# Kernel optimization log

Hardware: AMD Instinct MI355X
Metric: run time of the kernel (lower is better)

Reference implementation:

```python
import jax, jax.numpy as jnp
import numpy as np

EMBED = 1024
MLP = 2048
N_EXPERTS = 8
TOP_K = 2


def setup_inputs() -> dict:
    key = jax.random.key(0)
    ks = jax.random.split(key, 5)
    scale_e = 1.0 / np.sqrt(EMBED)
    scale_m = 1.0 / np.sqrt(MLP)
    x = jax.random.normal(ks[0], (4, 2048, EMBED), dtype=jnp.float32)
    gate_w = jax.random.normal(ks[1], (EMBED, N_EXPERTS), dtype=jnp.float32) * scale_e
    w1 = jax.random.normal(ks[2], (N_EXPERTS, EMBED, MLP), dtype=jnp.float32) * scale_e
    w3 = jax.random.normal(ks[3], (N_EXPERTS, EMBED, MLP), dtype=jnp.float32) * scale_e
    w2 = jax.random.normal(ks[4], (N_EXPERTS, MLP, EMBED), dtype=jnp.float32) * scale_m
    return {"x": x, "gate_w": gate_w, "w1": w1, "w2": w2, "w3": w3}


def reference(x, gate_w, w1, w2, w3):
    B, S, D = x.shape
    xf = x.reshape(-1, D)  # [T, D] tokens
    # Router: softmax over experts, top-k select, renormalize selected weights
    router_logits = xf @ gate_w                      # [T, E]
    routing_weights = jax.nn.softmax(router_logits, axis=-1)
    sel_w, sel_e = jax.lax.top_k(routing_weights, TOP_K)  # [T, K]
    sel_w = sel_w / jnp.sum(sel_w, axis=-1, keepdims=True)
    out = jnp.zeros_like(xf)
    # Loop over the small fixed expert set; tokens not routed to expert e get
    # coefficient 0, matching the gather/scatter-add combine of the original.
    for e in range(N_EXPERTS):
        coef = jnp.sum(jnp.where(sel_e == e, sel_w, 0.0), axis=-1)  # [T]
        h = jax.nn.silu(xf @ w1[e]) * (xf @ w3[e])                  # [T, Mlp] SwiGLU
        out = out + coef[:, None] * (h @ w2[e])                     # [T, D]
    return out.reshape(B, S, D)
```

## Files before the change

kernel.cpp:

```cpp
#include <hip/hip_runtime.h>

#define EMBED 1024
#define MLP   2048
#define NE    8
#define NTOK  8192
#define RMAX  (2*NTOK + NE*128)

typedef _Float16 f16x8 __attribute__((ext_vector_type(8)));
typedef _Float16 f16x4 __attribute__((ext_vector_type(4)));
typedef float    f32x4 __attribute__((ext_vector_type(4)));

__device__ __forceinline__ void async_copy16(const void* g, void* l) {
  __builtin_amdgcn_global_load_lds(
      (const __attribute__((address_space(1))) unsigned int*)g,
      (__attribute__((address_space(3))) unsigned int*)l, 16, 0, 0);
}

__global__ __launch_bounds__(256) void router_kernel(
    const float* __restrict__ x, const float* __restrict__ gw,
    int* __restrict__ sel_e, float* __restrict__ sel_w, int* __restrict__ counts)
{
  __shared__ float gwt[NE * EMBED];
  __shared__ int cnt[NE];
  int tid = threadIdx.x;
  for (int idx = tid; idx < NE * EMBED; idx += 256) {
    int i = idx >> 3, e = idx & 7;
    gwt[e * EMBED + i] = gw[idx];
  }
  if (tid < NE) cnt[tid] = 0;
  __syncthreads();

  int lane = tid & 63, wv = tid >> 6;
  int t = blockIdx.x * 4 + wv;
  const float4* xr = (const float4*)(x + (size_t)t * EMBED);
  const float4* gt4 = (const float4*)gwt;
  float acc[NE];
  #pragma unroll
  for (int e = 0; e < NE; ++e) acc[e] = 0.f;
  #pragma unroll
  for (int c = 0; c < 4; ++c) {
    float4 xv = xr[c * 64 + lane];
    #pragma unroll
    for (int e = 0; e < NE; ++e) {
      float4 gv = gt4[e * 256 + c * 64 + lane];
      acc[e] += xv.x * gv.x + xv.y * gv.y + xv.z * gv.z + xv.w * gv.w;
    }
  }
  #pragma unroll
  for (int off = 1; off < 64; off <<= 1) {
    #pragma unroll
    for (int e = 0; e < NE; ++e) acc[e] += __shfl_xor(acc[e], off);
  }
  if (lane == 0) {
    int e0 = 0; float l0 = acc[0];
    #pragma unroll
    for (int e = 1; e < NE; ++e) if (acc[e] > l0) { l0 = acc[e]; e0 = e; }
    int e1 = -1; float l1 = -1e30f;
    #pragma unroll
    for (int e = 0; e < NE; ++e) if (e != e0 && acc[e] > l1) { l1 = acc[e]; e1 = e; }
    float w0 = 1.f / (1.f + expf(l1 - l0));
    sel_e[2 * t] = e0;     sel_w[2 * t] = w0;
    sel_e[2 * t + 1] = e1; sel_w[2 * t + 1] = 1.f - w0;
    atomicAdd(&cnt[e0], 1); atomicAdd(&cnt[e1], 1);
  }
  __syncthreads();
  if (tid < NE && cnt[tid]) atomicAdd(&counts[tid], cnt[tid]);
}

__global__ void offsets_kernel(const int* __restrict__ counts,
                               int* __restrict__ offs, int* __restrict__ cursor)
{
  if (threadIdx.x == 0) {
    int o = 0;
    for (int e = 0; e < NE; ++e) {
      offs[e] = o; cursor[e] = o;
      o += (counts[e] + 127) & ~127;
    }
    offs[NE] = o;
  }
}

__global__ __launch_bounds__(256) void assign_kernel(
    const int* __restrict__ sel_e, const float* __restrict__ sel_w,
    int* __restrict__ cursor, int* __restrict__ rowtok, float* __restrict__ rowcoef)
{
  int t = blockIdx.x * 256 + threadIdx.x;
  int lane = threadIdx.x & 63;
  #pragma unroll
  for (int k = 0; k < 2; ++k) {
    int e = sel_e[2 * t + k];
    float w = sel_w[2 * t + k];
    for (int xch = 0; xch < NE; ++xch) {
      unsigned long long m = __ballot(e == xch);
      if (e == xch) {
        int leader = __ffsll((unsigned long long)m) - 1;
        int base = 0;
        if (lane == leader) base = atomicAdd(&cursor[xch], (int)__popcll(m));
        base = __shfl(base, leader);
        int pos = base + (int)__popcll(m & ((1ull << lane) - 1));
        rowtok[pos] = t;
        rowcoef[pos] = w;
      }
    }
  }
}

__global__ __launch_bounds__(256) void gather_kernel(
    const float* __restrict__ x, const int* __restrict__ rowtok,
    _Float16* __restrict__ xg)
{
  int r = blockIdx.x;
  int tok = rowtok[r];
  int t4 = threadIdx.x * 4;
  _Float16* dst = xg + (size_t)r * EMBED + t4;
  if (tok >= 0) {
    float4 v = *(const float4*)(x + (size_t)tok * EMBED + t4);
    f16x4 h; h.x = (_Float16)v.x; h.y = (_Float16)v.y; h.z = (_Float16)v.z; h.w = (_Float16)v.w;
    *(f16x4*)dst = h;
  } else {
    f16x4 z = {(_Float16)0.f, (_Float16)0.f, (_Float16)0.f, (_Float16)0.f};
    *(f16x4*)dst = z;
  }
}

__global__ __launch_bounds__(256) void transpose_cast_kernel(
    const float* __restrict__ in, _Float16* __restrict__ out, int K, int N)
{
  const float* src = in + (size_t)blockIdx.z * K * N;
  _Float16* dst = out + (size_t)blockIdx.z * K * N;
  int k0 = blockIdx.x * 64, n0 = blockIdx.y * 64;
  __shared__ float tile[64][65];
  int t = threadIdx.x;
  int r = t >> 4, c4 = (t & 15) * 4;
  #pragma unroll
  for (int i = 0; i < 4; ++i) {
    float4 v = *(const float4*)(src + (size_t)(k0 + r + 16 * i) * N + n0 + c4);
    tile[r + 16 * i][c4 + 0] = v.x;
    tile[r + 16 * i][c4 + 1] = v.y;
    tile[r + 16 * i][c4 + 2] = v.z;
    tile[r + 16 * i][c4 + 3] = v.w;
  }
  __syncthreads();
  int kk8 = (t & 7) * 8, nIdx = t >> 3;
  #pragma unroll
  for (int i = 0; i < 2; ++i) {
    int n = nIdx + 32 * i;
    f16x8 h;
    #pragma unroll
    for (int j = 0; j < 8; ++j) h[j] = (_Float16)tile[kk8 + j][n];
    *(f16x8*)(dst + (size_t)(n0 + n) * K + k0 + kk8) = h;
  }
}

__device__ __forceinline__ int resolve_expert(const int* __restrict__ offs, int r0)
{
  int e = 0;
  #pragma unroll
  for (int q = 0; q < NE - 1; ++q) if (r0 >= offs[q + 1]) e = q + 1;
  return e;
}

__device__ __forceinline__ const _Float16* frag_addr(const _Float16* buf, int row, int quad)
{
  return buf + row * 32 + ((quad ^ ((row >> 1) & 3)) << 3);
}

__global__ __launch_bounds__(256, 2) void gemm1_kernel(
    const _Float16* __restrict__ xg, const _Float16* __restrict__ w1t,
    const _Float16* __restrict__ w3t, const float* __restrict__ rowcoef,
    const int* __restrict__ offs, _Float16* __restrict__ hb)
{
  int r0 = blockIdx.x * 128;
  if (r0 >= offs[NE]) return;
  int e = resolve_expert(offs, r0);
  int n0 = blockIdx.y * 128;
  const _Float16* B1 = w1t + (size_t)e * MLP * EMBED;
  const _Float16* B3 = w3t + (size_t)e * MLP * EMBED;

  __shared__ __align__(16) _Float16 As[128 * 32];
  __shared__ __align__(16) _Float16 Bs1[128 * 32];
  __shared__ __align__(16) _Float16 Bs3[128 * 32];

  int tid = threadIdx.x, lane = tid & 63, wv = tid >> 6;
  int wm = (wv & 1) << 6, wn = (wv >> 1) << 6;
  int l16 = lane & 15, quad = lane >> 4;

  f32x4 acc1[4][4], acc3[4][4];
  f32x4 z4 = {0.f, 0.f, 0.f, 0.f};
  #pragma unroll
  for (int i = 0; i < 4; ++i)
    #pragma unroll
    for (int j = 0; j < 4; ++j) { acc1[i][j] = z4; acc3[i][j] = z4; }

  for (int kk = 0; kk < EMBED; kk += 32) {
    __syncthreads();
    #pragma unroll
    for (int p = 0; p < 2; ++p) {
      int c = p * 256 + tid;
      int row = c >> 2, kqp = c & 3;
      int kql = kqp ^ ((row >> 1) & 3);
      size_t gof = (size_t)(r0 + row) * EMBED + kk + kql * 8;
      size_t gofB = (size_t)(n0 + row) * EMBED + kk + kql * 8;
      int lof = (p * 256 + wv * 64) * 8;
      async_copy16(xg + gof,  As  + lof);
      async_copy16(B1 + gofB, Bs1 + lof);
      async_copy16(B3 + gofB, Bs3 + lof);
    }
    __syncthreads();
    f16x8 af[4], b1f[4], b3f[4];
    #pragma unroll
    for (int i = 0; i < 4; ++i)
      af[i] = *(const f16x8*)frag_addr(As, wm + 16 * i + l16, quad);
    #pragma unroll
    for (int j = 0; j < 4; ++j) {
      b1f[j] = *(const f16x8*)frag_addr(Bs1, wn + 16 * j + l16, quad);
      b3f[j] = *(const f16x8*)frag_addr(Bs3, wn + 16 * j + l16, quad);
    }
    #pragma unroll
    for (int i = 0; i < 4; ++i)
      #pragma unroll
      for (int j = 0; j < 4; ++j) {
        acc1[i][j] = __builtin_amdgcn_mfma_f32_16x16x32_f16(af[i], b1f[j], acc1[i][j], 0, 0, 0);
        acc3[i][j] = __builtin_amdgcn_mfma_f32_16x16x32_f16(af[i], b3f[j], acc3[i][j], 0, 0, 0);
      }
  }

  #pragma unroll
  for (int i = 0; i < 4; ++i) {
    int mb = r0 + wm + 16 * i + quad * 4;
    float cf[4];
    #pragma unroll
    for (int rg = 0; rg < 4; ++rg) cf[rg] = rowcoef[mb + rg];
    #pragma unroll
    for (int j = 0; j < 4; ++j) {
      int col = n0 + wn + 16 * j + l16;
      #pragma unroll
      for (int rg = 0; rg < 4; ++rg) {
        float g = acc1[i][j][rg], u = acc3[i][j][rg];
        float h = g * u * cf[rg] / (1.f + __expf(-g));
        hb[(size_t)(mb + rg) * MLP + col] = (_Float16)h;
      }
    }
  }
}

__global__ __launch_bounds__(256, 2) void gemm2_kernel(
    const _Float16* __restrict__ hb, const _Float16* __restrict__ w2t,
    const int* __restrict__ rowtok, const int* __restrict__ offs,
    float* __restrict__ out)
{
  int r0 = blockIdx.x * 128;
  if (r0 >= offs[NE]) return;
  int e = resolve_expert(offs, r0);
  int n0 = blockIdx.y * 128;
  const _Float16* B = w2t + (size_t)e * EMBED * MLP;

  __shared__ __align__(16) _Float16 As[128 * 32];
  __shared__ __align__(16) _Float16 Bs[128 * 32];

  int tid = threadIdx.x, lane = tid & 63, wv = tid >> 6;
  int wm = (wv & 1) << 6, wn = (wv >> 1) << 6;
  int l16 = lane & 15, quad = lane >> 4;

  f32x4 acc[4][4];
  f32x4 z4 = {0.f, 0.f, 0.f, 0.f};
  #pragma unroll
  for (int i = 0; i < 4; ++i)
    #pragma unroll
    for (int j = 0; j < 4; ++j) acc[i][j] = z4;

  for (int kk = 0; kk < MLP; kk += 32) {
    __syncthreads();
    #pragma unroll
    for (int p = 0; p < 2; ++p) {
      int c = p * 256 + tid;
      int row = c >> 2, kqp = c & 3;
      int kql = kqp ^ ((row >> 1) & 3);
      size_t gofA = (size_t)(r0 + row) * MLP + kk + kql * 8;
      size_t gofB = (size_t)(n0 + row) * MLP + kk + kql * 8;
      int lof = (p * 256 + wv * 64) * 8;
      async_copy16(hb + gofA, As + lof);
      async_copy16(B  + gofB, Bs + lof);
    }
    __syncthreads();
    f16x8 af[4], bf[4];
    #pragma unroll
    for (int i = 0; i < 4; ++i)
      af[i] = *(const f16x8*)frag_addr(As, wm + 16 * i + l16, quad);
    #pragma unroll
    for (int j = 0; j < 4; ++j)
      bf[j] = *(const f16x8*)frag_addr(Bs, wn + 16 * j + l16, quad);
    #pragma unroll
    for (int i = 0; i < 4; ++i)
      #pragma unroll
      for (int j = 0; j < 4; ++j)
        acc[i][j] = __builtin_amdgcn_mfma_f32_16x16x32_f16(af[i], bf[j], acc[i][j], 0, 0, 0);
  }

  #pragma unroll
  for (int i = 0; i < 4; ++i) {
    int mb = r0 + wm + 16 * i + quad * 4;
    int tk[4];
    #pragma unroll
    for (int rg = 0; rg < 4; ++rg) tk[rg] = rowtok[mb + rg];
    #pragma unroll
    for (int j = 0; j < 4; ++j) {
      int col = n0 + wn + 16 * j + l16;
      #pragma unroll
      for (int rg = 0; rg < 4; ++rg)
        if (tk[rg] >= 0)
          atomicAdd(out + (size_t)tk[rg] * EMBED + col, acc[i][j][rg]);
    }
  }
}

extern "C" void kernel_launch(void* const* d_in, const int* in_sizes, int n_in,
                              void* d_out, int out_size, void* d_ws, size_t ws_size,
                              hipStream_t stream)
{
  (void)in_sizes; (void)n_in; (void)ws_size;
  const float* x  = (const float*)d_in[0];
  const float* gw = (const float*)d_in[1];
  const float* w1 = (const float*)d_in[2];
  const float* w2 = (const float*)d_in[3];
  const float* w3 = (const float*)d_in[4];
  float* out = (float*)d_out;
  char* ws = (char*)d_ws;

  size_t o = 0;
  auto alloc = [&](size_t bytes) { size_t r = o; o = (o + bytes + 255) & ~255ULL; return r; };
  const size_t wbytes = (size_t)NE * MLP * EMBED * 2;
  _Float16* w1t = (_Float16*)(ws + alloc(wbytes));
  _Float16* w3t = (_Float16*)(ws + alloc(wbytes));
  _Float16* w2t = (_Float16*)(ws + alloc(wbytes));
  _Float16* xg  = (_Float16*)(ws + alloc((size_t)RMAX * EMBED * 2));
  _Float16* hb  = (_Float16*)(ws + alloc((size_t)RMAX * MLP * 2));
  int*   rowtok  = (int*)(ws + alloc((size_t)RMAX * 4));
  float* rowcoef = (float*)(ws + alloc((size_t)RMAX * 4));
  int*   sel_e   = (int*)(ws + alloc((size_t)2 * NTOK * 4));
  float* sel_w   = (float*)(ws + alloc((size_t)2 * NTOK * 4));
  int*   meta    = (int*)(ws + alloc(256));
  int* counts = meta;
  int* offs   = meta + 8;
  int* cursor = meta + 17;

  hipMemsetAsync(out, 0, (size_t)out_size * 4, stream);
  hipMemsetAsync(meta, 0, 256, stream);
  hipMemsetAsync(rowtok, 0xFF, (size_t)RMAX * 4, stream);
  hipMemsetAsync(rowcoef, 0, (size_t)RMAX * 4, stream);

  transpose_cast_kernel<<<dim3(EMBED / 64, MLP / 64, NE), 256, 0, stream>>>(w1, w1t, EMBED, MLP);
  transpose_cast_kernel<<<dim3(EMBED / 64, MLP / 64, NE), 256, 0, stream>>>(w3, w3t, EMBED, MLP);
  transpose_cast_kernel<<<dim3(MLP / 64, EMBED / 64, NE), 256, 0, stream>>>(w2, w2t, MLP, EMBED);

  router_kernel<<<NTOK / 4, 256, 0, stream>>>(x, gw, sel_e, sel_w, counts);
  offsets_kernel<<<1, 64, 0, stream>>>(counts, offs, cursor);
  assign_kernel<<<NTOK / 256, 256, 0, stream>>>(sel_e, sel_w, cursor, rowtok, rowcoef);
  gather_kernel<<<RMAX, 256, 0, stream>>>(x, rowtok, xg);

  gemm1_kernel<<<dim3(RMAX / 128, MLP / 128), 256, 0, stream>>>(xg, w1t, w3t, rowcoef, offs, hb);
  gemm2_kernel<<<dim3(RMAX / 128, EMBED / 128), 256, 0, stream>>>(hb, w2t, rowtok, offs, out);
}
```

Before: 678.4 us.

## Load GEMM A operands directly from global, deepen K tile, replace atomics with combine

The expert GEMMs now read A fragments straight from global memory into registers instead of staging them in LDS, and the K step grows to 64 with a new XOR swizzle for the B tiles. The atomic scatter-add in the second GEMM is replaced by an fp16 store into a per-row buffer, followed by a combine kernel that sums each token's two expert rows through an inverse index. The three weight transpose launches are merged into one. This is meant to remove atomic contention, the output memset and LDS traffic for A, at the cost of uncoalesced global A loads, an extra pass over the output, and fp16 rounding of the partial expert outputs.

Result: slower. 709.6 us (+4.6%).

```diff
diff --git a/kernel.cpp b/kernel.cpp
--- a/kernel.cpp
+++ b/kernel.cpp
@@ -5,6 +5,7 @@
 #define NE    8
 #define NTOK  8192
 #define RMAX  (2*NTOK + NE*128)
+#define BK    64
 
 typedef _Float16 f16x8 __attribute__((ext_vector_type(8)));
 typedef _Float16 f16x4 __attribute__((ext_vector_type(4)));
@@ -82,7 +83,8 @@
 
 __global__ __launch_bounds__(256) void assign_kernel(
     const int* __restrict__ sel_e, const float* __restrict__ sel_w,
-    int* __restrict__ cursor, int* __restrict__ rowtok, float* __restrict__ rowcoef)
+    int* __restrict__ cursor, int* __restrict__ rowtok, float* __restrict__ rowcoef,
+    int* __restrict__ inv)
 {
   int t = blockIdx.x * 256 + threadIdx.x;
   int lane = threadIdx.x & 63;
@@ -100,6 +102,7 @@
         int pos = base + (int)__popcll(m & ((1ull << lane) - 1));
         rowtok[pos] = t;
         rowcoef[pos] = w;
+        inv[2 * t + k] = pos;
       }
     }
   }
@@ -123,22 +126,34 @@
   }
 }
 
-__global__ __launch_bounds__(256) void transpose_cast_kernel(
-    const float* __restrict__ in, _Float16* __restrict__ out, int K, int N)
-{
-  const float* src = in + (size_t)blockIdx.z * K * N;
-  _Float16* dst = out + (size_t)blockIdx.z * K * N;
-  int k0 = blockIdx.x * 64, n0 = blockIdx.y * 64;
-  __shared__ float tile[64][65];
+__global__ __launch_bounds__(256) void transpose_all_kernel(
+    const float* __restrict__ w1, const float* __restrict__ w3,
+    const float* __restrict__ w2, _Float16* __restrict__ w1t,
+    _Float16* __restrict__ w3t, _Float16* __restrict__ w2t)
+{
+  int id = blockIdx.x;
+  int mat = id >> 12;
+  int rr = id & 4095;
+  int e = rr >> 9, tile = rr & 511;
+  const float* src; _Float16* dst; int K, N;
+  if (mat == 0)      { src = w1; dst = w1t; K = EMBED; N = MLP; }
+  else if (mat == 1) { src = w3; dst = w3t; K = EMBED; N = MLP; }
+  else               { src = w2; dst = w2t; K = MLP;   N = EMBED; }
+  int nx = K >> 6;
+  int k0 = (tile % nx) * 64, n0 = (tile / nx) * 64;
+  src += (size_t)e * K * N;
+  dst += (size_t)e * K * N;
+
+  __shared__ float tilebuf[64][65];
   int t = threadIdx.x;
   int r = t >> 4, c4 = (t & 15) * 4;
   #pragma unroll
   for (int i = 0; i < 4; ++i) {
     float4 v = *(const float4*)(src + (size_t)(k0 + r + 16 * i) * N + n0 + c4);
-    tile[r + 16 * i][c4 + 0] = v.x;
-    tile[r + 16 * i][c4 + 1] = v.y;
-    tile[r + 16 * i][c4 + 2] = v.z;
-    tile[r + 16 * i][c4 + 3] = v.w;
+    tilebuf[r + 16 * i][c4 + 0] = v.x;
+    tilebuf[r + 16 * i][c4 + 1] = v.y;
+    tilebuf[r + 16 * i][c4 + 2] = v.z;
+    tilebuf[r + 16 * i][c4 + 3] = v.w;
   }
   __syncthreads();
   int kk8 = (t & 7) * 8, nIdx = t >> 3;
@@ -147,7 +162,7 @@
     int n = nIdx + 32 * i;
     f16x8 h;
     #pragma unroll
-    for (int j = 0; j < 8; ++j) h[j] = (_Float16)tile[kk8 + j][n];
+    for (int j = 0; j < 8; ++j) h[j] = (_Float16)tilebuf[kk8 + j][n];
     *(f16x8*)(dst + (size_t)(n0 + n) * K + k0 + kk8) = h;
   }
 }
@@ -160,9 +175,10 @@
   return e;
 }
 
-__device__ __forceinline__ const _Float16* frag_addr(const _Float16* buf, int row, int quad)
-{
-  return buf + row * 32 + ((quad ^ ((row >> 1) & 3)) << 3);
+__device__ __forceinline__ const _Float16* bfrag_addr(const _Float16* buf, int row,
+                                                      int s, int quad)
+{
+  return buf + row * BK + ((((s << 2) + quad) ^ (row & 7)) << 3);
 }
 
 __global__ __launch_bounds__(256, 2) void gemm1_kernel(
@@ -177,14 +193,18 @@
   const _Float16* B1 = w1t + (size_t)e * MLP * EMBED;
   const _Float16* B3 = w3t + (size_t)e * MLP * EMBED;
 
-  __shared__ __align__(16) _Float16 As[128 * 32];
-  __shared__ __align__(16) _Float16 Bs1[128 * 32];
-  __shared__ __align__(16) _Float16 Bs3[128 * 32];
+  __shared__ __align__(16) _Float16 Bs1[128 * BK];
+  __shared__ __align__(16) _Float16 Bs3[128 * BK];
 
   int tid = threadIdx.x, lane = tid & 63, wv = tid >> 6;
   int wm = (wv & 1) << 6, wn = (wv >> 1) << 6;
   int l16 = lane & 15, quad = lane >> 4;
 
+  const _Float16* Arow[4];
+  #pragma unroll
+  for (int i = 0; i < 4; ++i)
+    Arow[i] = xg + (size_t)(r0 + wm + 16 * i + l16) * EMBED + quad * 8;
+
   f32x4 acc1[4][4], acc3[4][4];
   f32x4 z4 = {0.f, 0.f, 0.f, 0.f};
   #pragma unroll
@@ -192,37 +212,42 @@
     #pragma unroll
     for (int j = 0; j < 4; ++j) { acc1[i][j] = z4; acc3[i][j] = z4; }
 
-  for (int kk = 0; kk < EMBED; kk += 32) {
+  for (int kk = 0; kk < EMBED; kk += BK) {
     __syncthreads();
     #pragma unroll
-    for (int p = 0; p < 2; ++p) {
+    for (int p = 0; p < 4; ++p) {
       int c = p * 256 + tid;
-      int row = c >> 2, kqp = c & 3;
-      int kql = kqp ^ ((row >> 1) & 3);
-      size_t gof = (size_t)(r0 + row) * EMBED + kk + kql * 8;
-      size_t gofB = (size_t)(n0 + row) * EMBED + kk + kql * 8;
+      int row = c >> 3, cp = c & 7;
+      int cl = cp ^ (row & 7);
+      size_t gof = (size_t)(n0 + row) * EMBED + kk + cl * 8;
       int lof = (p * 256 + wv * 64) * 8;
-      async_copy16(xg + gof,  As  + lof);
-      async_copy16(B1 + gofB, Bs1 + lof);
-      async_copy16(B3 + gofB, Bs3 + lof);
-    }
+      async_copy16(B1 + gof, Bs1 + lof);
+      async_copy16(B3 + gof, Bs3 + lof);
+    }
+    f16x8 af[2][4];
+    #pragma unroll
+    for (int s = 0; s < 2; ++s)
+      #pragma unroll
+      for (int i = 0; i < 4; ++i)
+        af[s][i] = *(const f16x8*)(Arow[i] + kk + s * 32);
     __syncthreads();
-    f16x8 af[4], b1f[4], b3f[4];
-    #pragma unroll
-    for (int i = 0; i < 4; ++i)
-      af[i] = *(const f16x8*)frag_addr(As, wm + 16 * i + l16, quad);
-    #pragma unroll
-    for (int j = 0; j < 4; ++j) {
-      b1f[j] = *(const f16x8*)frag_addr(Bs1, wn + 16 * j + l16, quad);
-      b3f[j] = *(const f16x8*)frag_addr(Bs3, wn + 16 * j + l16, quad);
-    }
-    #pragma unroll
-    for (int i = 0; i < 4; ++i)
+    #pragma unroll
+    for (int s = 0; s < 2; ++s) {
+      f16x8 b1f[4], b3f[4];
       #pragma unroll
       for (int j = 0; j < 4; ++j) {
-        acc1[i][j] = __builtin_amdgcn_mfma_f32_16x16x32_f16(af[i], b1f[j], acc1[i][j], 0, 0, 0);
-        acc3[i][j] = __builtin_amdgcn_mfma_f32_16x16x32_f16(af[i], b3f[j], acc3[i][j], 0, 0, 0);
+        int row = wn + 16 * j + l16;
+        b1f[j] = *(const f16x8*)bfrag_addr(Bs1, row, s, quad);
+        b3f[j] = *(const f16x8*)bfrag_addr(Bs3, row, s, quad);
       }
+      #pragma unroll
+      for (int i = 0; i < 4; ++i)
+        #pragma unroll
+        for (int j = 0; j < 4; ++j) {
+          acc1[i][j] = __builtin_amdgcn_mfma_f32_16x16x32_f16(af[s][i], b1f[j], acc1[i][j], 0, 0, 0);
+          acc3[i][j] = __builtin_amdgcn_mfma_f32_16x16x32_f16(af[s][i], b3f[j], acc3[i][j], 0, 0, 0);
+        }
+    }
   }
 
   #pragma unroll
@@ -246,8 +271,7 @@
 
 __global__ __launch_bounds__(256, 2) void gemm2_kernel(
     const _Float16* __restrict__ hb, const _Float16* __restrict__ w2t,
-    const int* __restrict__ rowtok, const int* __restrict__ offs,
-    float* __restrict__ out)
+    const int* __restrict__ offs, _Float16* __restrict__ hb2)
 {
   int r0 = blockIdx.x * 128;
   if (r0 >= offs[NE]) return;
@@ -255,13 +279,17 @@
   int n0 = blockIdx.y * 128;
   const _Float16* B = w2t + (size_t)e * EMBED * MLP;
 
-  __shared__ __align__(16) _Float16 As[128 * 32];
-  __shared__ __align__(16) _Float16 Bs[128 * 32];
+  __shared__ __align__(16) _Float16 Bs[128 * BK];
 
   int tid = threadIdx.x, lane = tid & 63, wv = tid >> 6;
   int wm = (wv & 1) << 6, wn = (wv >> 1) << 6;
   int l16 = lane & 15, quad = lane >> 4;
 
+  const _Float16* Arow[4];
+  #pragma unroll
+  for (int i = 0; i < 4; ++i)
+    Arow[i] = hb + (size_t)(r0 + wm + 16 * i + l16) * MLP + quad * 8;
+
   f32x4 acc[4][4];
   f32x4 z4 = {0.f, 0.f, 0.f, 0.f};
   #pragma unroll
@@ -269,56 +297,73 @@
     #pragma unroll
     for (int j = 0; j < 4; ++j) acc[i][j] = z4;
 
-  for (int kk = 0; kk < MLP; kk += 32) {
+  for (int kk = 0; kk < MLP; kk += BK) {
     __syncthreads();
     #pragma unroll
-    for (int p = 0; p < 2; ++p) {
+    for (int p = 0; p < 4; ++p) {
       int c = p * 256 + tid;
-      int row = c >> 2, kqp = c & 3;
-      int kql = kqp ^ ((row >> 1) & 3);
-      size_t gofA = (size_t)(r0 + row) * MLP + kk + kql * 8;
-      size_t gofB = (size_t)(n0 + row) * MLP + kk + kql * 8;
+      int row = c >> 3, cp = c & 7;
+      int cl = cp ^ (row & 7);
+      size_t gof = (size_t)(n0 + row) * MLP + kk + cl * 8;
       int lof = (p * 256 + wv * 64) * 8;
-      async_copy16(hb + gofA, As + lof);
-      async_copy16(B  + gofB, Bs + lof);
-    }
+      async_copy16(B + gof, Bs + lof);
+    }
+    f16x8 af[2][4];
+    #pragma unroll
+    for (int s = 0; s < 2; ++s)
+      #pragma unroll
+      for (int i = 0; i < 4; ++i)
+        af[s][i] = *(const f16x8*)(Arow[i] + kk + s * 32);
     __syncthreads();
-    f16x8 af[4], bf[4];
-    #pragma unroll
-    for (int i = 0; i < 4; ++i)
-      af[i] = *(const f16x8*)frag_addr(As, wm + 16 * i + l16, quad);
-    #pragma unroll
-    for (int j = 0; j < 4; ++j)
-      bf[j] = *(const f16x8*)frag_addr(Bs, wn + 16 * j + l16, quad);
-    #pragma unroll
-    for (int i = 0; i < 4; ++i)
+    #pragma unroll
+    for (int s = 0; s < 2; ++s) {
+      f16x8 bf[4];
       #pragma unroll
       for (int j = 0; j < 4; ++j)
-        acc[i][j] = __builtin_amdgcn_mfma_f32_16x16x32_f16(af[i], bf[j], acc[i][j], 0, 0, 0);
+        bf[j] = *(const f16x8*)bfrag_addr(Bs, wn + 16 * j + l16, s, quad);
+      #pragma unroll
+      for (int i = 0; i < 4; ++i)
+        #pragma unroll
+        for (int j = 0; j < 4; ++j)
+          acc[i][j] = __builtin_amdgcn_mfma_f32_16x16x32_f16(af[s][i], bf[j], acc[i][j], 0, 0, 0);
+    }
   }
 
   #pragma unroll
   for (int i = 0; i < 4; ++i) {
     int mb = r0 + wm + 16 * i + quad * 4;
-    int tk[4];
-    #pragma unroll
-    for (int rg = 0; rg < 4; ++rg) tk[rg] = rowtok[mb + rg];
     #pragma unroll
     for (int j = 0; j < 4; ++j) {
       int col = n0 + wn + 16 * j + l16;
       #pragma unroll
       for (int rg = 0; rg < 4; ++rg)
-        if (tk[rg] >= 0)
-          atomicAdd(out + (size_t)tk[rg] * EMBED + col, acc[i][j][rg]);
-    }
-  }
+        hb2[(size_t)(mb + rg) * EMBED + col] = (_Float16)acc[i][j][rg];
+    }
+  }
+}
+
+__global__ __launch_bounds__(256) void combine_kernel(
+    const _Float16* __restrict__ hb2, const int* __restrict__ inv,
+    float* __restrict__ out)
+{
+  int t = blockIdx.x;
+  int d = threadIdx.x * 4;
+  int p0 = inv[2 * t], p1 = inv[2 * t + 1];
+  f16x4 a = *(const f16x4*)(hb2 + (size_t)p0 * EMBED + d);
+  f16x4 b = *(const f16x4*)(hb2 + (size_t)p1 * EMBED + d);
+  float4 r;
+  r.x = (float)a.x + (float)b.x;
+  r.y = (float)a.y + (float)b.y;
+  r.z = (float)a.z + (float)b.z;
+  r.w = (float)a.w + (float)b.w;
+  *(float4*)(out + (size_t)t * EMBED + d) = r;
 }
 
 extern "C" void kernel_launch(void* const* d_in, const int* in_sizes, int n_in,
                               void* d_out, int out_size, void* d_ws, size_t ws_size,
                               hipStream_t stream)
 {
-  (void)in_sizes; (void)n_in; (void)ws_size;
+  (void)in_sizes; (void)n_in; (void)ws_size; (void)out_size;
   const float* x  = (const float*)d_in[0];
   const float* gw = (const float*)d_in[1];
   const float* w1 = (const float*)d_in[2];
@@ -339,25 +384,25 @@
   float* rowcoef = (float*)(ws + alloc((size_t)RMAX * 4));
   int*   sel_e   = (int*)(ws + alloc((size_t)2 * NTOK * 4));
   float* sel_w   = (float*)(ws + alloc((size_t)2 * NTOK * 4));
+  int*   inv     = (int*)(ws + alloc((size_t)2 * NTOK * 4));
   int*   meta    = (int*)(ws + alloc(256));
   int* counts = meta;
   int* offs   = meta + 8;
   int* cursor = meta + 17;
-
-  hipMemsetAsync(out, 0, (size_t)out_size * 4, stream);
+  _Float16* hb2 = xg;
+
   hipMemsetAsync(meta, 0, 256, stream);
   hipMemsetAsync(rowtok, 0xFF, (size_t)RMAX * 4, stream);
   hipMemsetAsync(rowcoef, 0, (size_t)RMAX * 4, stream);
 
-  transpose_cast_kernel<<<dim3(EMBED / 64, MLP / 64, NE), 256, 0, stream>>>(w1, w1t, EMBED, MLP);
-  transpose_cast_kernel<<<dim3(EMBED / 64, MLP / 64, NE), 256, 0, stream>>>(w3, w3t, EMBED, MLP);
-  transpose_cast_kernel<<<dim3(MLP / 64, EMBED / 64, NE), 256, 0, stream>>>(w2, w2t, MLP, EMBED);
+  transpose_all_kernel<<<3 * 4096, 256, 0, stream>>>(w1, w3, w2, w1t, w3t, w2t);
 
   router_kernel<<<NTOK / 4, 256, 0, stream>>>(x, gw, sel_e, sel_w, counts);
   offsets_kernel<<<1, 64, 0, stream>>>(counts, offs, cursor);
-  assign_kernel<<<NTOK / 256, 256, 0, stream>>>(sel_e, sel_w, cursor, rowtok, rowcoef);
+  assign_kernel<<<NTOK / 256, 256, 0, stream>>>(sel_e, sel_w, cursor, rowtok, rowcoef, inv);
   gather_kernel<<<RMAX, 256, 0, stream>>>(x, rowtok, xg);
 
   gemm1_kernel<<<dim3(RMAX / 128, MLP / 128), 256, 0, stream>>>(xg, w1t, w3t, rowcoef, offs, hb);
-  gemm2_kernel<<<dim3(RMAX / 128, EMBED / 128), 256, 0, stream>>>(hb, w2t, rowtok, offs, out);
-}
+  gemm2_kernel<<<dim3(RMAX / 128, EMBED / 128), 256, 0, stream>>>(hb, w2t, offs, hb2);
+  combine_kernel<<<NTOK, 256, 0, stream>>>(hb2, inv, out);
+}
```
